# Optimization experiments

Measured on AMD Instinct MI355X. Metric: run time of the kernel, lower is better.

Reference implementation:

```python
import jax, jax.numpy as jnp
import numpy as np
import math

EMB = 128
KH = 256
VH = 256
NP_ = 32
B, T = 64, 1024


def setup_inputs() -> dict:
    key = jax.random.key(0)
    ks = jax.random.split(key, 12)
    s = 1.0 / math.sqrt(EMB)
    sk = 1.0 / math.sqrt(KH)
    return {
        "x": jax.random.normal(ks[0], (B, T, EMB), dtype=jnp.float32),
        "mask": jnp.ones((B, 1, T), dtype=bool),
        "person_idxs": jax.random.randint(ks[1], (B,), 0, NP_),
        # nn.Linear weights are [out, in]
        "Wk": jax.random.uniform(ks[2], (KH, EMB), jnp.float32, -s, s),
        "Wq": jax.random.uniform(ks[3], (KH, EMB), jnp.float32, -s, s),
        "Wv": jax.random.uniform(ks[4], (VH, EMB), jnp.float32, -s, s),
        # stacked per-person Linear(KH, KH) weights/biases (routing table)
        "PK_W": jax.random.uniform(ks[5], (NP_, KH, KH), jnp.float32, -sk, sk),
        "PK_b": jax.random.uniform(ks[6], (NP_, KH), jnp.float32, -sk, sk),
        "PQ_W": jax.random.uniform(ks[7], (NP_, KH, KH), jnp.float32, -sk, sk),
        "PQ_b": jax.random.uniform(ks[8], (NP_, KH), jnp.float32, -sk, sk),
    }


def reference(x, mask, person_idxs, Wk, Wq, Wv, PK_W, PK_b, PQ_W, PQ_b):
    # shared projections: [b,t,kh]
    k0 = jnp.einsum("bte,he->bth", x, Wk)
    q0 = jnp.einsum("bte,he->bth", x, Wq)
    v = jnp.einsum("bte,he->bth", x, Wv)  # [b,t,vh]
    # routed per-person linear: gather weights by person id, batched matmul
    keys = jnp.einsum("bth,boh->bto", k0, PK_W[person_idxs]) + PK_b[person_idxs][:, None, :]
    queries = jnp.einsum("bth,boh->bto", q0, PQ_W[person_idxs]) + PQ_b[person_idxs][:, None, :]
    queries = queries / math.sqrt(KH)
    dot = jnp.einsum("btd,bsd->bts", queries, keys)  # [b,t,t]
    dot = jnp.where(mask, dot, -jnp.inf)  # mask [b,1,t] broadcasts over query axis
    attention = jax.nn.softmax(dot, axis=-1)
    context = jnp.einsum("bts,bsd->btd", attention, v)  # [b,t,vh]
    return context
```

## Files before the change

kernel.cpp:

```cpp
#include <hip/hip_runtime.h>
#include <hip/hip_bf16.h>
#include <stdint.h>

#define EMB 128
#define KH  256
#define TT  1024

typedef __bf16 bf16x8 __attribute__((ext_vector_type(8)));
typedef float  f32x4  __attribute__((ext_vector_type(4)));
typedef float  f32x16 __attribute__((ext_vector_type(16)));
typedef unsigned short u16x8 __attribute__((ext_vector_type(8)));

__device__ inline unsigned short f2b(float f) {
  unsigned u = __builtin_bit_cast(unsigned, f);
  u += 0x7FFF + ((u >> 16) & 1);
  return (unsigned short)(u >> 16);
}

__device__ inline f32x4 mfma16(bf16x8 a, bf16x8 b, f32x4 c) {
  return __builtin_amdgcn_mfma_f32_16x16x32_bf16(a, b, c, 0, 0, 0);
}
__device__ inline f32x16 mfma32(bf16x8 a, bf16x8 b, f32x16 c) {
  return __builtin_amdgcn_mfma_f32_32x32x16_bf16(a, b, c, 0, 0, 0);
}
__device__ inline f32x16 zero16() {
  f32x16 z;
  #pragma unroll
  for (int i = 0; i < 16; ++i) z[i] = 0.f;
  return z;
}
__device__ inline void gload_lds16(const void* g, void* l) {
  __builtin_amdgcn_global_load_lds(
      (const __attribute__((address_space(1))) unsigned int*)g,
      (__attribute__((address_space(3))) unsigned int*)l, 16, 0, 0);
}

__global__ __launch_bounds__(256) void combine_kernel(
    const float* __restrict__ Wk, const float* __restrict__ Wq,
    const float* __restrict__ Wv,
    const float* __restrict__ PKW, const float* __restrict__ PQW,
    unsigned short* __restrict__ MK, unsigned short* __restrict__ MQ,
    unsigned short* __restrict__ Wvb)
{
  int bx = blockIdx.x;
  int tid = threadIdx.x;
  if (bx >= 256) {
    for (int i = tid; i < KH * EMB; i += 256) Wvb[i] = f2b(Wv[i]);
    return;
  }
  int mat = bx >> 7;
  int p   = (bx >> 2) & 31;
  int o0  = (bx & 3) * 64;
  const float* W  = mat ? Wq : Wk;
  const float* PW = (mat ? PQW : PKW) + (size_t)p * KH * KH;
  unsigned short* M = (mat ? MQ : MK) + (size_t)(p * KH + o0) * EMB;

  __shared__ float Wl[64 * 128];
  __shared__ float Pl[64 * 65];

  int e0 = (tid & 31) * 4;
  int og = tid >> 5;
  float acc[8][4] = {};

  for (int ht = 0; ht < KH; ht += 64) {
    __syncthreads();
    for (int i = tid; i < 64 * 128; i += 256)
      Wl[i] = W[(size_t)(ht + (i >> 7)) * EMB + (i & 127)];
    for (int i = tid; i < 64 * 64; i += 256) {
      int o = i >> 6, hh = i & 63;
      Pl[o * 65 + hh] = PW[(size_t)(o0 + o) * KH + ht + hh];
    }
    __syncthreads();
    for (int hh = 0; hh < 64; ++hh) {
      float4 wv4 = *(const float4*)&Wl[hh * 128 + e0];
      #pragma unroll
      for (int u = 0; u < 8; ++u) {
        float pv = Pl[(og + 8 * u) * 65 + hh];
        acc[u][0] += pv * wv4.x; acc[u][1] += pv * wv4.y;
        acc[u][2] += pv * wv4.z; acc[u][3] += pv * wv4.w;
      }
    }
  }
  float sc = mat ? 0.0625f : 1.0f;
  #pragma unroll
  for (int u = 0; u < 8; ++u) {
    int o = og + 8 * u;
    ushort4 st;
    st.x = f2b(acc[u][0] * sc); st.y = f2b(acc[u][1] * sc);
    st.z = f2b(acc[u][2] * sc); st.w = f2b(acc[u][3] * sc);
    *(ushort4*)&M[(size_t)o * EMB + e0] = st;
  }
}

__global__ __launch_bounds__(256) void proj_kernel(
    const float* __restrict__ x, const int* __restrict__ pidx,
    const unsigned short* __restrict__ MK, const unsigned short* __restrict__ MQ,
    const unsigned short* __restrict__ Wvb,
    const float* __restrict__ PKb, const float* __restrict__ PQb,
    unsigned short* __restrict__ Q, unsigned short* __restrict__ K,
    unsigned short* __restrict__ Vt)
{
  __shared__ unsigned short xl[64 * 128];
  __shared__ unsigned short vtl[4][4096];
  int b  = blockIdx.x >> 4;
  int t0 = (blockIdx.x & 15) * 64;
  int p  = pidx[b];
  int tid = threadIdx.x;

  for (int i = tid; i < 2048; i += 256) {
    int row = i >> 5, eg = i & 31;
    float4 v = *(const float4*)&x[(size_t)(b * TT + t0 + row) * EMB + eg * 4];
    int e = eg * 4;
    int sl = (e >> 3) ^ (row & 7);
    ushort4 s;
    s.x = f2b(v.x); s.y = f2b(v.y); s.z = f2b(v.z); s.w = f2b(v.w);
    *(ushort4*)&xl[row * 128 + sl * 8 + (e & 7)] = s;
  }
  __syncthreads();

  int w = tid >> 6, l = tid & 63, lr = l & 15, lg = l >> 4;

  bf16x8 a[4];
  {
    int row = 16 * w + lr;
    #pragma unroll
    for (int s = 0; s < 4; ++s) {
      int sl = (s * 4 + lg) ^ (row & 7);
      a[s] = *(const bf16x8*)&xl[row * 128 + sl * 8];
    }
  }

  #pragma unroll
  for (int mat = 0; mat < 2; ++mat) {
    const unsigned short* M = (mat ? MQ : MK) + (size_t)p * KH * EMB;
    const float* bias = (mat ? PQb : PKb) + (size_t)p * KH;
    unsigned short* Out = mat ? Q : K;
    float bscale = mat ? 0.0625f : 1.0f;
    f32x4 acc[16];
    #pragma unroll
    for (int i = 0; i < 16; ++i) acc[i] = (f32x4){0.f, 0.f, 0.f, 0.f};
    #pragma unroll
    for (int cf = 0; cf < 16; ++cf) {
      const unsigned short* Mp = M + (size_t)(cf * 16 + lr) * EMB + lg * 8;
      #pragma unroll
      for (int s = 0; s < 4; ++s) {
        bf16x8 bv = *(const bf16x8*)(Mp + 32 * s);
        acc[cf] = mfma16(a[s], bv, acc[cf]);
      }
    }
    unsigned short* vt = &vtl[w][0];
    #pragma unroll
    for (int cf = 0; cf < 16; ++cf) {
      int o = cf * 16 + lr;
      float bvv = bias[o] * bscale;
      int chunk = o >> 3;
      #pragma unroll
      for (int r = 0; r < 4; ++r) {
        int trow = lg * 4 + r;
        vt[trow * 256 + ((chunk ^ (trow & 7)) * 8) + (o & 7)] = f2b(acc[cf][r] + bvv);
      }
    }
    asm volatile("s_waitcnt lgkmcnt(0)" ::: "memory");
    __builtin_amdgcn_sched_barrier(0);
    int c = l & 31, rs = l >> 5;
    #pragma unroll
    for (int i = 0; i < 8; ++i) {
      int trow = i * 2 + rs;
      u16x8 v = *(const u16x8*)(vt + trow * 256 + c * 8);
      int g = c ^ (trow & 7);
      *(u16x8*)&Out[(size_t)(b * TT + t0 + w * 16 + trow) * KH + g * 8] = v;
    }
  }

  {
    f32x16 dummy; (void)dummy;
    f32x4 acc[16];
    #pragma unroll
    for (int i = 0; i < 16; ++i) acc[i] = (f32x4){0.f, 0.f, 0.f, 0.f};
    #pragma unroll
    for (int s = 0; s < 4; ++s) {
      bf16x8 bv[4];
      #pragma unroll
      for (int cf = 0; cf < 4; ++cf) {
        int row = cf * 16 + lr;
        int sl = (s * 4 + lg) ^ (row & 7);
        bv[cf] = *(const bf16x8*)&xl[row * 128 + sl * 8];
      }
      #pragma unroll
      for (int rf = 0; rf < 4; ++rf) {
        int d = 64 * w + rf * 16 + lr;
        bf16x8 av = *(const bf16x8*)&Wvb[(size_t)d * EMB + 32 * s + lg * 8];
        #pragma unroll
        for (int cf = 0; cf < 4; ++cf)
          acc[rf * 4 + cf] = mfma16(av, bv[cf], acc[rf * 4 + cf]);
      }
    }
    unsigned short* vt = &vtl[w][0];
    #pragma unroll
    for (int rf = 0; rf < 4; ++rf) {
      #pragma unroll
      for (int cf = 0; cf < 4; ++cf) {
        #pragma unroll
        for (int r = 0; r < 4; ++r) {
          int dl = rf * 16 + lg * 4 + r;
          int tc = cf * 16 + lr;
          int chunk = tc >> 3;
          vt[dl * 64 + ((chunk ^ (dl & 7)) * 8) + (tc & 7)] = f2b(acc[rf * 4 + cf][r]);
        }
      }
    }
    asm volatile("s_waitcnt lgkmcnt(0)" ::: "memory");
    __builtin_amdgcn_sched_barrier(0);
    int c8 = l & 7, r8 = l >> 3;
    #pragma unroll
    for (int i = 0; i < 8; ++i) {
      int dr = i * 8 + r8;
      u16x8 v = *(const u16x8*)(vt + dr * 64 + c8 * 8);
      int g = c8 ^ (dr & 7);
      *(u16x8*)&Vt[(size_t)(b * KH + w * 64 + dr) * TT + t0 + g * 8] = v;
    }
  }
}

__global__ __launch_bounds__(512, 2) void attn_kernel(
    const unsigned short* __restrict__ Q, const unsigned short* __restrict__ K,
    const unsigned short* __restrict__ Vt, float* __restrict__ out)
{
  __shared__ unsigned short Kl[2][64 * 256];
  __shared__ unsigned short Vl[2][128 * 64];
  __shared__ unsigned short Pl[8][32 * 64];

  int j = blockIdx.x;
  int xcd = j & 7, slot = j >> 3;
  int qt = slot & 3, dh = (slot >> 2) & 1, b = xcd * 8 + (slot >> 3);

  int tid = threadIdx.x;
  int w = tid >> 6, l = tid & 63;
  int q31 = l & 31, h = l >> 5, rk = q31 & 7;

  const unsigned short* Kb = K + (size_t)b * TT * KH;
  const unsigned short* Vb = Vt + (size_t)(b * KH + dh * 128) * TT;

  bf16x8 qa[16];
  {
    const unsigned short* Qp =
        Q + (size_t)(b * TT + qt * 256 + w * 32 + q31) * KH + h * 8;
    #pragma unroll
    for (int s = 0; s < 16; ++s)
      qa[s] = *(const bf16x8*)(Qp + s * 16);
  }

  bf16x8 ones;
  #pragma unroll
  for (int i = 0; i < 8; ++i) ones[i] = (__bf16)1.0f;

  f32x16 acc[4];
  #pragma unroll
  for (int i = 0; i < 4; ++i) acc[i] = zero16();
  f32x16 sacc = zero16();

  auto stage = [&](int sb, int k0) {
    unsigned short* Kd = &Kl[sb][0];
    unsigned short* Vd = &Vl[sb][0];
    int c = l & 31, rs = l >> 5;
    #pragma unroll
    for (int i = 0; i < 4; ++i) {
      int r = w * 8 + i * 2 + rs;
      gload_lds16(Kb + (size_t)(k0 + r) * KH + ((c ^ (r & 7)) * 8),
                  Kd + (w * 8 + i * 2) * 256);
    }
    int c8 = l & 7, r8 = l >> 3;
    #pragma unroll
    for (int i = 0; i < 2; ++i) {
      int dr = w * 16 + i * 8 + r8;
      gload_lds16(Vb + (size_t)dr * TT + k0 + ((c8 ^ (dr & 7)) * 8),
                  Vd + (w * 16 + i * 8) * 64);
    }
  };

  stage(0, 0);
  int buf = 0;
  unsigned short* myp = &Pl[w][0];

  for (int kt = 0; kt < 16; ++kt) {
    if (kt < 15) {
      stage(buf ^ 1, (kt + 1) * 64);
      asm volatile("s_waitcnt vmcnt(6)" ::: "memory");
    } else {
      asm volatile("s_waitcnt vmcnt(0)" ::: "memory");
    }
    __builtin_amdgcn_s_barrier();
    __builtin_amdgcn_sched_barrier(0);

    const unsigned short* Kcur = &Kl[buf][0];
    const unsigned short* Vcur = &Vl[buf][0];

    f32x16 s0 = zero16(), s1 = zero16();
    #pragma unroll
    for (int s = 0; s < 16; ++s) {
      int ch = 2 * s + h;
      bf16x8 b0 = *(const bf16x8*)(Kcur + q31 * 256 + ((ch ^ rk) * 8));
      bf16x8 b1 = *(const bf16x8*)(Kcur + (32 + q31) * 256 + ((ch ^ rk) * 8));
      s0 = mfma32(qa[s], b0, s0);
      s1 = mfma32(qa[s], b1, s1);
    }

    #pragma unroll
    for (int r = 0; r < 16; ++r) {
      int qloc = (r & 3) + 8 * (r >> 2) + 4 * h;
      int qk7 = qloc & 7;
      int ch0 = q31 >> 3;
      myp[qloc * 64 + ((ch0 ^ qk7) * 8) + (q31 & 7)] = f2b(__expf(s0[r]));
      myp[qloc * 64 + (((4 + ch0) ^ qk7) * 8) + (q31 & 7)] = f2b(__expf(s1[r]));
    }
    asm volatile("s_waitcnt lgkmcnt(0)" ::: "memory");
    __builtin_amdgcn_sched_barrier(0);

    #pragma unroll
    for (int s2 = 0; s2 < 4; ++s2) {
      int ch = 2 * s2 + h;
      bf16x8 pa = *(const bf16x8*)(myp + q31 * 64 + ((ch ^ rk) * 8));
      #pragma unroll
      for (int dt = 0; dt < 4; ++dt) {
        bf16x8 vb = *(const bf16x8*)(Vcur + (dt * 32 + q31) * 64 + ((ch ^ rk) * 8));
        acc[dt] = mfma32(pa, vb, acc[dt]);
      }
      sacc = mfma32(pa, ones, sacc);
    }
    __builtin_amdgcn_s_barrier();
    __builtin_amdgcn_sched_barrier(0);
    buf ^= 1;
  }

  float* op = out + (size_t)(b * TT + qt * 256 + w * 32) * KH + dh * 128;
  #pragma unroll
  for (int r = 0; r < 16; ++r) {
    int qloc = (r & 3) + 8 * (r >> 2) + 4 * h;
    float inv = 1.0f / sacc[r];
    #pragma unroll
    for (int dt = 0; dt < 4; ++dt)
      op[(size_t)qloc * KH + dt * 32 + q31] = acc[dt][r] * inv;
  }
}

extern "C" void kernel_launch(void* const* d_in, const int* in_sizes, int n_in,
                              void* d_out, int out_size, void* d_ws, size_t ws_size,
                              hipStream_t stream) {
  (void)in_sizes; (void)n_in; (void)out_size; (void)ws_size;
  const float* x    = (const float*)d_in[0];
  const int*   pidx = (const int*)d_in[2];
  const float* Wk   = (const float*)d_in[3];
  const float* Wq   = (const float*)d_in[4];
  const float* Wv   = (const float*)d_in[5];
  const float* PKW  = (const float*)d_in[6];
  const float* PKb  = (const float*)d_in[7];
  const float* PQW  = (const float*)d_in[8];
  const float* PQb  = (const float*)d_in[9];
  float* out = (float*)d_out;

  char* ws = (char*)d_ws;
  unsigned short* MK  = (unsigned short*)(ws);
  unsigned short* MQ  = (unsigned short*)(ws + (2u << 20));
  unsigned short* Wvb = (unsigned short*)(ws + (4u << 20));
  unsigned short* Qb  = (unsigned short*)(ws + (8u << 20));
  unsigned short* Kb  = (unsigned short*)(ws + (40u << 20));
  unsigned short* Vt  = (unsigned short*)(ws + (72u << 20));

  combine_kernel<<<257, 256, 0, stream>>>(Wk, Wq, Wv, PKW, PQW, MK, MQ, Wvb);
  proj_kernel<<<1024, 256, 0, stream>>>(x, pidx, MK, MQ, Wvb, PKb, PQb, Qb, Kb, Vt);
  attn_kernel<<<512, 512, 0, stream>>>(Qb, Kb, Vt, out);
}
```

Measured before the change: 241.6 us.

## Compute full value width per attention block to stop recomputing QK scores

The attention kernel previously split the value dimension into two halves across blocks, so each block recomputed the full QK^T and exp for its query tile. Now each block covers all 256 value columns with 8 accumulators and half as many blocks, and it processes the key tile in two 32-key halves with a smaller P buffer. The row sum moves from an MFMA against a ones vector to a per-lane float accumulation followed by a wave shuffle reduction. This removes the duplicated score work and K loads. In exchange it uses more accumulator registers and launches only 256 blocks, which may lower occupancy and leave compute units idle.

```diff
diff --git a/kernel.cpp b/kernel.cpp
--- a/kernel.cpp
+++ b/kernel.cpp
@@ -173,7 +173,6 @@
   }
 
   {
-    f32x16 dummy; (void)dummy;
     f32x4 acc[16];
     #pragma unroll
     for (int i = 0; i < 16; ++i) acc[i] = (f32x4){0.f, 0.f, 0.f, 0.f};
@@ -227,119 +226,123 @@
     const unsigned short* __restrict__ Vt, float* __restrict__ out)
 {
   __shared__ unsigned short Kl[2][64 * 256];
-  __shared__ unsigned short Vl[2][128 * 64];
-  __shared__ unsigned short Pl[8][32 * 64];
-
-  int j = blockIdx.x;
-  int xcd = j & 7, slot = j >> 3;
-  int qt = slot & 3, dh = (slot >> 2) & 1, b = xcd * 8 + (slot >> 3);
+  __shared__ unsigned short Vl[2][64 * 256];
+  __shared__ unsigned short Ptl[8][32 * 32];
+
+  int bx = blockIdx.x;
+  int slot = bx >> 3;
+  int b  = (bx & 7) * 8 + (slot & 7);
+  int qt = slot >> 3;
 
   int tid = threadIdx.x;
   int w = tid >> 6, l = tid & 63;
-  int q31 = l & 31, h = l >> 5, rk = q31 & 7;
-
-  const unsigned short* Kb = K + (size_t)b * TT * KH;
-  const unsigned short* Vb = Vt + (size_t)(b * KH + dh * 128) * TT;
+  int q31 = l & 31, h = l >> 5;
+
+  const unsigned short* Kg = K + (size_t)b * TT * KH;
+  const unsigned short* Vg = Vt + (size_t)b * KH * TT;
+  int qbase = qt * 256 + w * 32;
 
   bf16x8 qa[16];
   {
-    const unsigned short* Qp =
-        Q + (size_t)(b * TT + qt * 256 + w * 32 + q31) * KH + h * 8;
-    #pragma unroll
-    for (int s = 0; s < 16; ++s)
-      qa[s] = *(const bf16x8*)(Qp + s * 16);
-  }
-
-  bf16x8 ones;
-  #pragma unroll
-  for (int i = 0; i < 8; ++i) ones[i] = (__bf16)1.0f;
-
-  f32x16 acc[4];
-  #pragma unroll
-  for (int i = 0; i < 4; ++i) acc[i] = zero16();
-  f32x16 sacc = zero16();
+    const unsigned short* Qp = Q + (size_t)(b * TT + qbase + q31) * KH + h * 8;
+    #pragma unroll
+    for (int s = 0; s < 16; ++s) qa[s] = *(const bf16x8*)(Qp + s * 16);
+  }
+
+  f32x16 acc[8];
+  #pragma unroll
+  for (int i = 0; i < 8; ++i) acc[i] = zero16();
+  float psum[16];
+  #pragma unroll
+  for (int i = 0; i < 16; ++i) psum[i] = 0.f;
 
   auto stage = [&](int sb, int k0) {
-    unsigned short* Kd = &Kl[sb][0];
-    unsigned short* Vd = &Vl[sb][0];
-    int c = l & 31, rs = l >> 5;
     #pragma unroll
     for (int i = 0; i < 4; ++i) {
-      int r = w * 8 + i * 2 + rs;
-      gload_lds16(Kb + (size_t)(k0 + r) * KH + ((c ^ (r & 7)) * 8),
-                  Kd + (w * 8 + i * 2) * 256);
-    }
-    int c8 = l & 7, r8 = l >> 3;
-    #pragma unroll
-    for (int i = 0; i < 2; ++i) {
-      int dr = w * 16 + i * 8 + r8;
-      gload_lds16(Vb + (size_t)dr * TT + k0 + ((c8 ^ (dr & 7)) * 8),
-                  Vd + (w * 16 + i * 8) * 64);
+      int m = (w * 4 + i) * 64 + l;
+      int row = m >> 5;
+      int c = (m & 31) ^ (row & 31);
+      gload_lds16(Kg + (size_t)(k0 + row) * KH + c * 8,
+                  &Kl[sb][(w * 4 + i) * 512]);
+    }
+    #pragma unroll
+    for (int i = 0; i < 4; ++i) {
+      int m = (w * 4 + i) * 64 + l;
+      int lrow = m >> 5;
+      int u = (m & 31) ^ (lrow & 31);
+      int seg = u >> 3, c = u & 7;
+      gload_lds16(Vg + (size_t)(seg * 64 + lrow) * TT + k0 + c * 8,
+                  &Vl[sb][(w * 4 + i) * 512]);
     }
   };
 
   stage(0, 0);
-  int buf = 0;
-  unsigned short* myp = &Pl[w][0];
+  unsigned short* myp = &Ptl[w][0];
 
   for (int kt = 0; kt < 16; ++kt) {
+    int cur = kt & 1;
     if (kt < 15) {
-      stage(buf ^ 1, (kt + 1) * 64);
-      asm volatile("s_waitcnt vmcnt(6)" ::: "memory");
+      stage(cur ^ 1, (kt + 1) * 64);
+      asm volatile("s_waitcnt vmcnt(8)" ::: "memory");
     } else {
       asm volatile("s_waitcnt vmcnt(0)" ::: "memory");
     }
     __builtin_amdgcn_s_barrier();
     __builtin_amdgcn_sched_barrier(0);
-
-    const unsigned short* Kcur = &Kl[buf][0];
-    const unsigned short* Vcur = &Vl[buf][0];
-
-    f32x16 s0 = zero16(), s1 = zero16();
-    #pragma unroll
-    for (int s = 0; s < 16; ++s) {
-      int ch = 2 * s + h;
-      bf16x8 b0 = *(const bf16x8*)(Kcur + q31 * 256 + ((ch ^ rk) * 8));
-      bf16x8 b1 = *(const bf16x8*)(Kcur + (32 + q31) * 256 + ((ch ^ rk) * 8));
-      s0 = mfma32(qa[s], b0, s0);
-      s1 = mfma32(qa[s], b1, s1);
-    }
-
-    #pragma unroll
-    for (int r = 0; r < 16; ++r) {
-      int qloc = (r & 3) + 8 * (r >> 2) + 4 * h;
-      int qk7 = qloc & 7;
-      int ch0 = q31 >> 3;
-      myp[qloc * 64 + ((ch0 ^ qk7) * 8) + (q31 & 7)] = f2b(__expf(s0[r]));
-      myp[qloc * 64 + (((4 + ch0) ^ qk7) * 8) + (q31 & 7)] = f2b(__expf(s1[r]));
-    }
-    asm volatile("s_waitcnt lgkmcnt(0)" ::: "memory");
-    __builtin_amdgcn_sched_barrier(0);
-
-    #pragma unroll
-    for (int s2 = 0; s2 < 4; ++s2) {
-      int ch = 2 * s2 + h;
-      bf16x8 pa = *(const bf16x8*)(myp + q31 * 64 + ((ch ^ rk) * 8));
-      #pragma unroll
-      for (int dt = 0; dt < 4; ++dt) {
-        bf16x8 vb = *(const bf16x8*)(Vcur + (dt * 32 + q31) * 64 + ((ch ^ rk) * 8));
-        acc[dt] = mfma32(pa, vb, acc[dt]);
-      }
-      sacc = mfma32(pa, ones, sacc);
+    const unsigned short* Kc = &Kl[cur][0];
+    const unsigned short* Vc = &Vl[cur][0];
+
+    #pragma unroll
+    for (int kh = 0; kh < 2; ++kh) {
+      f32x16 st = zero16();
+      #pragma unroll
+      for (int s = 0; s < 16; ++s) {
+        bf16x8 kb = *(const bf16x8*)(Kc + (kh * 32 + q31) * 256 +
+                                     (((2 * s + h) ^ q31) << 3));
+        st = mfma32(qa[s], kb, st);
+      }
+      #pragma unroll
+      for (int r = 0; r < 16; ++r) {
+        float p = __expf(st[r]);
+        psum[r] += p;
+        int row = (r & 3) + 8 * (r >> 2) + 4 * h;
+        int sl = (q31 >> 3) ^ (row & 3);
+        myp[row * 32 + sl * 8 + (q31 & 7)] = f2b(p);
+      }
+      asm volatile("s_waitcnt lgkmcnt(0)" ::: "memory");
+      __builtin_amdgcn_sched_barrier(0);
+      #pragma unroll
+      for (int s2 = 0; s2 < 2; ++s2) {
+        bf16x8 pa = *(const bf16x8*)(myp + q31 * 32 +
+                                     (((2 * s2 + h) ^ (q31 & 3)) << 3));
+        #pragma unroll
+        for (int dt = 0; dt < 8; ++dt) {
+          int lrow = (dt & 1) * 32 + q31;
+          int u = (dt >> 1) * 8 + 4 * kh + 2 * s2 + h;
+          bf16x8 vb = *(const bf16x8*)(Vc + lrow * 256 + ((u ^ q31) << 3));
+          acc[dt] = mfma32(pa, vb, acc[dt]);
+        }
+      }
     }
     __builtin_amdgcn_s_barrier();
     __builtin_amdgcn_sched_barrier(0);
-    buf ^= 1;
-  }
-
-  float* op = out + (size_t)(b * TT + qt * 256 + w * 32) * KH + dh * 128;
+  }
+
+  #pragma unroll
+  for (int m = 1; m < 32; m <<= 1) {
+    #pragma unroll
+    for (int r = 0; r < 16; ++r)
+      psum[r] += __shfl_xor(psum[r], m, 64);
+  }
+
+  float* ob = out + (size_t)(b * TT + qbase) * KH;
   #pragma unroll
   for (int r = 0; r < 16; ++r) {
-    int qloc = (r & 3) + 8 * (r >> 2) + 4 * h;
-    float inv = 1.0f / sacc[r];
-    #pragma unroll
-    for (int dt = 0; dt < 4; ++dt)
-      op[(size_t)qloc * KH + dt * 32 + q31] = acc[dt][r] * inv;
+    int kk = (r & 3) + 8 * (r >> 2) + 4 * h;
+    float inv = 1.0f / psum[r];
+    #pragma unroll
+    for (int dt = 0; dt < 8; ++dt)
+      ob[(size_t)kk * KH + dt * 32 + q31] = acc[dt][r] * inv;
   }
 }
 
@@ -368,5 +371,5 @@
 
   combine_kernel<<<257, 256, 0, stream>>>(Wk, Wq, Wv, PKW, PQW, MK, MQ, Wvb);
   proj_kernel<<<1024, 256, 0, stream>>>(x, pidx, MK, MQ, Wvb, PKb, PQb, Qb, Kb, Vt);
-  attn_kernel<<<512, 512, 0, stream>>>(Qb, Kb, Vt, out);
-}
+  attn_kernel<<<256, 512, 0, stream>>>(Qb, Kb, Vt, out);
+}
```

After: 343.7 us. 42.2% more time.
